# Kernel tuning notes

Hardware: AMD Instinct MI355X
Metric: run time of the kernel (lower is better)

The kernel has to match this reference:

```python
import jax, jax.numpy as jnp
import numpy as np

B, T, D, H = 2, 2048, 1024, 16
HD = D // H


def sinusoidal_rel_pe(seq_len, d_model, dtype=jnp.float32):
    # Relative positions T-1 .. 0 (reversed), standard sin/cos interleave.
    pos = jnp.arange(seq_len - 1, -1, -1, dtype=jnp.float32)[:, None]  # [T,1]
    div = jnp.exp(-jnp.log(jnp.float32(10000.0)) * jnp.arange(0, d_model, 2, dtype=jnp.float32) / d_model)
    pe = jnp.zeros((seq_len, d_model), dtype=jnp.float32)
    pe = pe.at[:, 0::2].set(jnp.sin(pos * div))
    pe = pe.at[:, 1::2].set(jnp.cos(pos * div))
    return pe.astype(dtype)


def relative_to_absolute(x):
    # x: [B,H,T,L] with L == T. Music-Transformer skew trick.
    b, h, t1, l = x.shape
    x = jnp.pad(x, ((0, 0), (0, 0), (0, 0), (1, 0)))          # pad left of last dim
    x = x.reshape(b, h, -1)
    x = jnp.pad(x, ((0, 0), (0, 0), (l - t1, 0)))
    x = x.reshape(b, h, 1 + t1, l)
    return x[:, :, 1:]


def setup_inputs() -> dict:
    key = jax.random.key(0)
    k1, k2, k3 = jax.random.split(key, 3)
    x = jax.random.normal(k1, (B, T, D), dtype=jnp.float32)
    # causal mask: True where attention is disallowed (j > i)
    mask = jnp.triu(jnp.ones((T, T), dtype=bool), k=1)[None, None]
    mask = jnp.broadcast_to(mask, (B, 1, T, T))
    Wqkv = jax.random.normal(k2, (D, 3 * D), dtype=jnp.float32) * 0.02
    Wout = jax.random.normal(k3, (D, D), dtype=jnp.float32) * 0.02
    bout = jnp.zeros((D,), dtype=jnp.float32)
    return {"x": x, "mask": mask, "Wqkv": Wqkv, "Wout": Wout, "bout": bout}


def reference(x, mask, Wqkv, Wout, bout):
    b, t, d = x.shape
    scale = jnp.sqrt(jnp.float32(HD)).astype(x.dtype)
    qkv = x @ Wqkv                                  # [B,T,3D]
    q, k, v = jnp.split(qkv, 3, axis=-1)
    E = sinusoidal_rel_pe(t, d, x.dtype)            # [T,D], constant rel bias
    q = q.reshape(b, t, H, HD).transpose(0, 2, 1, 3)   # [B,H,T,hd]
    k = k.reshape(b, t, H, HD).transpose(0, 2, 1, 3)
    v = v.reshape(b, t, H, HD).transpose(0, 2, 1, 3)
    Eh = E.reshape(t, H, HD).transpose(1, 0, 2)        # [H,T,hd]
    att_k = jnp.einsum('bhqd,bhkd->bhqk', q, k)
    att_e = relative_to_absolute(jnp.einsum('bhqd,hkd->bhqk', q, Eh))
    score = (att_k + att_e) / scale
    score = jnp.where(mask, -jnp.inf, score)
    score = jax.nn.softmax(score, axis=-1)          # dropout is identity (eval)
    ctx = jnp.einsum('bhqk,bhkd->bhqd', score, v)
    ctx = ctx.transpose(0, 2, 1, 3).reshape(b, t, d)
    out = ctx @ Wout + bout
    return (out, score)
```

## Files before the change

### kernel.cpp

```cpp
#include <hip/hip_runtime.h>

typedef __bf16 bf16x8 __attribute__((ext_vector_type(8)));
typedef float f32x4 __attribute__((ext_vector_type(4)));
typedef float f32x16 __attribute__((ext_vector_type(16)));

#define B_ 2
#define T_ 2048
#define D_ 1024
#define H_ 16

__device__ __forceinline__ ushort f2bf(float f) {
  union { float f; unsigned u; } v; v.f = f;
  unsigned u = v.u;
  return (ushort)((u + 0x7FFFu + ((u >> 16) & 1u)) >> 16);
}

__device__ __forceinline__ void g2l16(const void* g, void* l) {
  __builtin_amdgcn_global_load_lds(
      (const __attribute__((address_space(1))) unsigned int*)g,
      (__attribute__((address_space(3))) unsigned int*)l, 16, 0, 0);
}

__global__ __launch_bounds__(256) void cvt_kernel(const float* __restrict__ in,
                                                  ushort* __restrict__ out) {
  int i = (blockIdx.x * 256 + threadIdx.x) * 4;
  float4 v = *(const float4*)(in + i);
  ushort4 o;
  o.x = f2bf(v.x); o.y = f2bf(v.y); o.z = f2bf(v.z); o.w = f2bf(v.w);
  *(ushort4*)(out + i) = o;
}

__global__ void transpose_cvt(const float* __restrict__ in, ushort* __restrict__ out,
                              int R, int C) {
  __shared__ float tile[32][33];
  int bx = blockIdx.x * 32, by = blockIdx.y * 32;
  int tx = threadIdx.x, ty = threadIdx.y;
  for (int i = 0; i < 32; i += 8)
    tile[ty + i][tx] = in[(size_t)(by + ty + i) * C + (bx + tx)];
  __syncthreads();
  for (int i = 0; i < 32; i += 8)
    out[(size_t)(bx + ty + i) * R + (by + tx)] = f2bf(tile[tx][ty + i]);
}

__global__ __launch_bounds__(256) void gemm_bf16(
    const ushort* __restrict__ A, const ushort* __restrict__ BT,
    float* __restrict__ C, const float* __restrict__ bias,
    int M, int N, int K) {
  __shared__ alignas(16) ushort As[2][4096];
  __shared__ alignas(16) ushort Bs[2][4096];
  int tid = threadIdx.x;
  int wave = tid >> 6, lane = tid & 63;
  int l16 = lane & 15, lhi = lane >> 4;
  int m0 = blockIdx.y * 128, n0 = blockIdx.x * 128;
  int wr = (wave >> 1) * 64, wc = (wave & 1) * 64;
  int srow = lane >> 2, sch = lane & 3;

  f32x4 acc[4][4] = {};

  auto stage = [&](int kk, int buf) {
    for (int i = 0; i < 2; ++i) {
      int rg = i * 4 + wave;
      g2l16(A + (size_t)(m0 + rg * 16 + srow) * K + kk + sch * 8, &As[buf][rg * 512]);
      g2l16(BT + (size_t)(n0 + rg * 16 + srow) * K + kk + sch * 8, &Bs[buf][rg * 512]);
    }
  };

  stage(0, 0);
  int buf = 0;
  for (int kk = 0; kk < K; kk += 32) {
    __syncthreads();
    if (kk + 32 < K) stage(kk + 32, buf ^ 1);
    const ushort* Asb = As[buf];
    const ushort* Bsb = Bs[buf];
    bf16x8 af[4], bfr[4];
    for (int f = 0; f < 4; ++f)
      af[f] = *(const bf16x8*)(Asb + (wr + f * 16 + l16) * 32 + lhi * 8);
    for (int f = 0; f < 4; ++f)
      bfr[f] = *(const bf16x8*)(Bsb + (wc + f * 16 + l16) * 32 + lhi * 8);
    for (int fm = 0; fm < 4; ++fm)
      for (int fn = 0; fn < 4; ++fn)
        acc[fm][fn] = __builtin_amdgcn_mfma_f32_16x16x32_bf16(af[fm], bfr[fn], acc[fm][fn], 0, 0, 0);
    buf ^= 1;
  }
  for (int fm = 0; fm < 4; ++fm)
    for (int fn = 0; fn < 4; ++fn)
      for (int r = 0; r < 4; ++r) {
        int row = m0 + wr + fm * 16 + lhi * 4 + r;
        int col = n0 + wc + fn * 16 + l16;
        float v = acc[fm][fn][r];
        if (bias) v += bias[col];
        C[(size_t)row * N + col] = v;
      }
}

__global__ __launch_bounds__(256) void augment_kernel(
    const float* __restrict__ qkv,
    ushort* __restrict__ Qaug, ushort* __restrict__ Kaug, ushort* __restrict__ Vb) {
  int row = blockIdx.x;
  int b = row >> 11;
  int t = row & 2047;
  int tid = threadIdx.x;
  const float* src = qkv + (size_t)row * 3072;
  for (int i = 0; i < 4; ++i) {
    int idx = tid + i * 256;
    int h = idx >> 6, d = idx & 63;
    size_t obase = ((size_t)(b * H_ + h) * T_ + t);
    float q = src[idx];
    float k = src[1024 + idx];
    float v = src[2048 + idx];
    Qaug[obase * 128 + d] = f2bf(q * 0.125f);
    Kaug[obase * 128 + d] = f2bf(k);
    Vb[obase * 64 + d] = f2bf(v);
  }
  for (int i = 0; i < 2; ++i) {
    int idx = tid + i * 256;
    int h = idx >> 5, mm = idx & 31;
    int gdim = h * 64 + 2 * mm;
    float w = __expf(-9.2103403719761836f * (float)gdim * (1.0f / 1024.0f));
    float ang = w * (float)t;
    float si, co;
    __sincosf(ang, &si, &co);
    float qs = src[h * 64 + 2 * mm], qc = src[h * 64 + 2 * mm + 1];
    size_t obase = ((size_t)(b * H_ + h) * T_ + t);
    Qaug[obase * 128 + 64 + 2 * mm]     = f2bf((qs * si + qc * co) * 0.125f);
    Qaug[obase * 128 + 64 + 2 * mm + 1] = f2bf((qc * si - qs * co) * 0.125f);
    Kaug[obase * 128 + 64 + 2 * mm]     = f2bf(co);
    Kaug[obase * 128 + 64 + 2 * mm + 1] = f2bf(si);
  }
}

__global__ __launch_bounds__(256) void transpose_v(const ushort* __restrict__ Vb,
                                                   ushort* __restrict__ Vt) {
  __shared__ ushort tile[64][72];
  int bh = blockIdx.y, t0 = blockIdx.x * 64;
  int tid = threadIdx.x;
  for (int i = 0; i < 2; ++i) {
    int e = tid + i * 256;
    int row = e >> 3, ch = e & 7;
    *(int4*)(&tile[row][ch * 8]) =
        *(const int4*)(Vb + ((size_t)bh * T_ + t0 + row) * 64 + ch * 8);
  }
  __syncthreads();
  for (int i = 0; i < 2; ++i) {
    int e = tid + i * 256;
    int d = e >> 3, ch = e & 7;
    union { int4 v; ushort u[8]; } pk;
    for (int u = 0; u < 8; ++u) pk.u[u] = tile[ch * 8 + u][d];
    *(int4*)(Vt + ((size_t)bh * 64 + d) * T_ + t0 + ch * 8) = pk.v;
  }
}

__device__ __forceinline__ int rowf32(int reg, int hi) {
  return (reg & 3) + 8 * (reg >> 2) + 4 * hi;
}

__global__ __launch_bounds__(256, 4) void denom_kernel(
    const ushort* __restrict__ Qaug,
    const ushort* __restrict__ Kaug,
    float* __restrict__ invlb) {
  int flat = blockIdx.y * 32 + blockIdx.x;
  int wg = (flat & 7) * 128 + (flat >> 3);
  int bh = wg >> 5;
  int qt = 31 - (wg & 31);
  int tid = threadIdx.x;
  int wave = tid >> 6, lane = tid & 63;
  int l31 = lane & 31, hi = lane >> 5;
  int r = wave >> 1, d = wave & 1;

  __shared__ alignas(16) ushort Ks[2][8192];
  __shared__ float sums[64];

  const ushort* Kbase = Kaug + (size_t)bh * T_ * 128;

  auto stageK = [&](int kt, int buf) {
    for (int i = 0; i < 4; ++i) {
      int rg = i * 4 + wave;
      int key = rg * 4 + (lane >> 4);
      const ushort* g = Kbase + ((size_t)(kt * 64 + key)) * 128 + (((lane & 15) ^ (key & 15)) << 3);
      g2l16(g, &Ks[buf][rg * 512]);
    }
  };

  bf16x8 qf[8];
  {
    const ushort* Qg = Qaug + ((size_t)bh * T_ + qt * 64 + r * 32 + l31) * 128;
    for (int ks = 0; ks < 8; ++ks)
      qf[ks] = *(const bf16x8*)(Qg + ks * 16 + hi * 8);
  }
  int key = d * 32 + l31;

  stageK(0, 0);
  asm volatile("s_waitcnt vmcnt(0)" ::: "memory");
  __builtin_amdgcn_s_barrier();
  float plsum[16];
  for (int i = 0; i < 16; ++i) plsum[i] = 0.f;

  for (int kt = 0; kt <= qt; ++kt) {
    int buf = kt & 1;
    if (kt < qt) stageK(kt + 1, buf ^ 1);
    __builtin_amdgcn_sched_barrier(0);
    const ushort* Kb = Ks[buf];
    f32x16 s = {};
    for (int ks = 0; ks < 8; ++ks) {
      int slot = (ks * 2 + hi) ^ (key & 15);
      bf16x8 kf = *(const bf16x8*)(Kb + key * 128 + (slot << 3));
      s = __builtin_amdgcn_mfma_f32_32x32x16_bf16(qf[ks], kf, s, 0, 0, 0);
    }
    if (kt == qt) {
      for (int reg = 0; reg < 16; ++reg)
        if (d * 32 + l31 > r * 32 + rowf32(reg, hi)) s[reg] = -1e30f;
    }
    for (int reg = 0; reg < 16; ++reg) plsum[reg] += __expf(s[reg]);
    if (kt < qt) {
      asm volatile("s_waitcnt vmcnt(0)" ::: "memory");
      __builtin_amdgcn_s_barrier();
    }
  }
  for (int reg = 0; reg < 16; ++reg) {
    float v = plsum[reg];
    for (int dd = 1; dd < 32; dd <<= 1) v += __shfl_xor(v, dd);
    plsum[reg] = v;
  }
  if (d == 1 && l31 == 0)
    for (int reg = 0; reg < 16; ++reg)
      sums[r * 32 + rowf32(reg, hi)] = plsum[reg];
  __syncthreads();
  if (d == 0 && l31 == 0)
    for (int reg = 0; reg < 16; ++reg) {
      int row = r * 32 + rowf32(reg, hi);
      invlb[(size_t)bh * T_ + qt * 64 + row] = 1.f / (plsum[reg] + sums[row]);
    }
}

__global__ __launch_bounds__(256) void attn2_kernel(
    const ushort* __restrict__ Qaug,
    const ushort* __restrict__ Kaug,
    const ushort* __restrict__ Vt,
    const float* __restrict__ invlb,
    float* __restrict__ score,
    ushort* __restrict__ ctxb) {
  int flat = blockIdx.y * 32 + blockIdx.x;
  int wg = (flat & 7) * 128 + (flat >> 3);
  int bh = wg >> 5;
  int qt = 31 - (wg & 31);
  int tid = threadIdx.x;
  int wave = tid >> 6, lane = tid & 63;
  int l31 = lane & 31, hi = lane >> 5;
  int r = wave >> 1, d = wave & 1;

  __shared__ alignas(16) ushort Ks[2][8192];
  __shared__ alignas(16) ushort Vs[2][4096];
  __shared__ alignas(16) ushort Ps[4096];

  const ushort* Kbase = Kaug + (size_t)bh * T_ * 128;
  const ushort* Vbase = Vt + (size_t)bh * 64 * T_;

  auto stageK = [&](int kt, int buf) {
    for (int i = 0; i < 4; ++i) {
      int rg = i * 4 + wave;
      int key = rg * 4 + (lane >> 4);
      const ushort* g = Kbase + ((size_t)(kt * 64 + key)) * 128 + (((lane & 15) ^ (key & 15)) << 3);
      g2l16(g, &Ks[buf][rg * 512]);
    }
  };
  auto stageV = [&](int kt, int buf) {
    for (int i = 0; i < 2; ++i) {
      int rg = i * 4 + wave;
      int dim = rg * 8 + (lane >> 3);
      const ushort* g = Vbase + (size_t)dim * T_ + kt * 64 + (((lane & 7) ^ (dim & 7)) << 3);
      g2l16(g, &Vs[buf][rg * 512]);
    }
  };

  bf16x8 qf[8];
  {
    const ushort* Qg = Qaug + ((size_t)bh * T_ + qt * 64 + r * 32 + l31) * 128;
    for (int ks = 0; ks < 8; ++ks)
      qf[ks] = *(const bf16x8*)(Qg + ks * 16 + hi * 8);
  }
  int key = d * 32 + l31;
  float4 iv[4];
  for (int g = 0; g < 4; ++g)
    iv[g] = *(const float4*)(invlb + (size_t)bh * T_ + qt * 64 + r * 32 + hi * 4 + g * 8);

  stageK(0, 0);
  stageV(0, 0);
  asm volatile("s_waitcnt vmcnt(0)" ::: "memory");
  __builtin_amdgcn_s_barrier();
  f32x16 cacc[2] = {};
  float* srow = score + ((size_t)bh * T_ + (size_t)qt * 64) * T_;

  for (int kt = 0; kt <= qt; ++kt) {
    int buf = kt & 1;
    if (kt < qt) { stageK(kt + 1, buf ^ 1); stageV(kt + 1, buf ^ 1); }
    __builtin_amdgcn_sched_barrier(0);
    const ushort* Kb = Ks[buf];
    f32x16 s = {};
    for (int ks = 0; ks < 8; ++ks) {
      int slot = (ks * 2 + hi) ^ (key & 15);
      bf16x8 kf = *(const bf16x8*)(Kb + key * 128 + (slot << 3));
      s = __builtin_amdgcn_mfma_f32_32x32x16_bf16(qf[ks], kf, s, 0, 0, 0);
    }
    if (kt == qt) {
      for (int reg = 0; reg < 16; ++reg)
        if (d * 32 + l31 > r * 32 + rowf32(reg, hi)) s[reg] = -1e30f;
    }
    for (int reg = 0; reg < 16; ++reg) {
      int row_loc = r * 32 + rowf32(reg, hi);
      float p = __expf(s[reg]) * iv[reg >> 2][reg & 3];
      srow[(size_t)row_loc * T_ + kt * 64 + key] = p;
      Ps[row_loc * 64 + ((((key >> 3)) ^ (row_loc & 7)) << 3) + (key & 7)] = f2bf(p);
    }
    asm volatile("s_waitcnt lgkmcnt(0)" ::: "memory");
    __builtin_amdgcn_sched_barrier(0);
    const ushort* Vb2 = Vs[buf];
    int rowA = r * 32 + l31;
    for (int ks2 = 0; ks2 < 2; ++ks2) {
      int chunkA = d * 4 + ks2 * 2 + hi;
      bf16x8 pa = *(const bf16x8*)(Ps + rowA * 64 + ((chunkA ^ (rowA & 7)) << 3));
      for (int b2 = 0; b2 < 2; ++b2) {
        int dim = b2 * 32 + l31;
        bf16x8 vb = *(const bf16x8*)(Vb2 + dim * 64 + ((chunkA ^ (dim & 7)) << 3));
        cacc[b2] = __builtin_amdgcn_mfma_f32_32x32x16_bf16(pa, vb, cacc[b2], 0, 0, 0);
      }
    }
    if (kt < qt) {
      asm volatile("s_waitcnt vmcnt(16)" ::: "memory");
      __builtin_amdgcn_s_barrier();
    }
  }

  {
    int row = tid >> 2, c16 = (tid & 3) * 16;
    f32x4 z = {0.f, 0.f, 0.f, 0.f};
    for (int kt = qt + 1; kt < 32; ++kt) {
      f32x4* dst = (f32x4*)(srow + (size_t)row * T_ + kt * 64 + c16);
      for (int u = 0; u < 4; ++u) dst[u] = z;
    }
  }

  __builtin_amdgcn_s_barrier();
  float* xch = (float*)Ks;
  if (d == 1) {
    for (int b2 = 0; b2 < 2; ++b2)
      for (int reg = 0; reg < 16; ++reg)
        xch[(r * 32 + rowf32(reg, hi)) * 64 + b2 * 32 + l31] = cacc[b2][reg];
  }
  __syncthreads();
  if (d == 0) {
    int b = bh >> 4, h = bh & 15;
    for (int b2 = 0; b2 < 2; ++b2)
      for (int reg = 0; reg < 16; ++reg) {
        int row_loc = r * 32 + rowf32(reg, hi);
        float v = cacc[b2][reg] + xch[row_loc * 64 + b2 * 32 + l31];
        int t = qt * 64 + row_loc;
        ctxb[((size_t)(b * T_ + t)) * 1024 + h * 64 + b2 * 32 + l31] = f2bf(v);
      }
  }
}

extern "C" void kernel_launch(void* const* d_in, const int* in_sizes, int n_in,
                              void* d_out, int out_size, void* d_ws, size_t ws_size,
                              hipStream_t stream) {
  const float* x    = (const float*)d_in[0];
  const float* Wqkv = (const float*)d_in[2];
  const float* Wout = (const float*)d_in[3];
  const float* bout = (const float*)d_in[4];

  char* ws = (char*)d_ws;
  ushort* xb    = (ushort*)(ws + 0);
  ushort* wqkvT = (ushort*)(ws + 8388608);
  ushort* woutT = (ushort*)(ws + 14680064);
  float*  qkv   = (float*) (ws + 16777216);
  ushort* Qaug  = (ushort*)(ws + 67108864);
  ushort* Kaug  = (ushort*)(ws + 83886080);
  ushort* Vb    = (ushort*)(ws + 100663296);
  ushort* ctxb  = (ushort*)(ws + 109051904);
  ushort* Vt    = (ushort*)(ws + 16777216);
  float*  invlb = (float*) (ws + 25165824);

  float* out   = (float*)d_out;
  float* score = out + (size_t)4194304;

  cvt_kernel<<<4096, 256, 0, stream>>>(x, xb);
  dim3 tb(32, 8);
  transpose_cvt<<<dim3(3072 / 32, 1024 / 32), tb, 0, stream>>>(Wqkv, wqkvT, 1024, 3072);
  transpose_cvt<<<dim3(1024 / 32, 1024 / 32), tb, 0, stream>>>(Wout, woutT, 1024, 1024);
  gemm_bf16<<<dim3(24, 32), 256, 0, stream>>>(xb, wqkvT, qkv, nullptr, 4096, 3072, 1024);
  augment_kernel<<<4096, 256, 0, stream>>>(qkv, Qaug, Kaug, Vb);
  transpose_v<<<dim3(32, 32), 256, 0, stream>>>(Vb, Vt);
  denom_kernel<<<dim3(32, 32), 256, 0, stream>>>(Qaug, Kaug, invlb);
  attn2_kernel<<<dim3(32, 32), 256, 0, stream>>>(Qaug, Kaug, Vt, invlb, score, ctxb);
  gemm_bf16<<<dim3(8, 32), 256, 0, stream>>>(ctxb, woutT, out, bout, 4096, 1024, 1024);
}
```

Before: 315.2 us.

## Fuse QKV augmentation into GEMM epilogue and precompute K trig columns

The QKV GEMM now writes bf16 Q (scaled, with the rotated relative-position half computed via shuffle-paired sin/cos), K and V directly in a token-major [B,T,H,128] layout. This removes the fp32 qkv intermediate and the separate augment kernel. A small kernel fills K's cos/sin columns independently of the GEMM. The attention kernels are re-indexed to read the new strided layout, so each K/Q row load now has a 4 KB stride between tokens instead of a contiguous per-head stream, and the GEMM epilogue takes on scattered 2-byte stores and sincos work.

```diff
diff --git a/kernel.cpp b/kernel.cpp
--- a/kernel.cpp
+++ b/kernel.cpp
@@ -8,6 +8,7 @@
 #define T_ 2048
 #define D_ 1024
 #define H_ 16
+#define NLOG4 -9.2103403719761836f
 
 __device__ __forceinline__ ushort f2bf(float f) {
   union { float f; unsigned u; } v; v.f = f;
@@ -42,10 +43,22 @@
     out[(size_t)(bx + ty + i) * R + (by + tx)] = f2bf(tile[tx][ty + i]);
 }
 
-__global__ __launch_bounds__(256) void gemm_bf16(
+__global__ __launch_bounds__(512) void fill_ktrig(ushort* __restrict__ Ka) {
+  int t = blockIdx.x;
+  int tid = threadIdx.x;
+  int h = tid >> 5, mm = tid & 31;
+  float w = __expf(NLOG4 * (float)(h * 64 + 2 * mm) * (1.0f / 1024.0f));
+  float si, co;
+  __sincosf(w * (float)t, &si, &co);
+  ushort2 pk;
+  pk.x = f2bf(co); pk.y = f2bf(si);
+  for (int b = 0; b < 2; ++b)
+    *(ushort2*)(Ka + ((size_t)(b * T_ + t) * 2048 + h * 128 + 64 + 2 * mm)) = pk;
+}
+
+__global__ __launch_bounds__(256) void gemm_qkv(
     const ushort* __restrict__ A, const ushort* __restrict__ BT,
-    float* __restrict__ C, const float* __restrict__ bias,
-    int M, int N, int K) {
+    ushort* __restrict__ Qa, ushort* __restrict__ Ka, ushort* __restrict__ Va) {
   __shared__ alignas(16) ushort As[2][4096];
   __shared__ alignas(16) ushort Bs[2][4096];
   int tid = threadIdx.x;
@@ -54,6 +67,7 @@
   int m0 = blockIdx.y * 128, n0 = blockIdx.x * 128;
   int wr = (wave >> 1) * 64, wc = (wave & 1) * 64;
   int srow = lane >> 2, sch = lane & 3;
+  const int K = 1024;
 
   f32x4 acc[4][4] = {};
 
@@ -82,6 +96,77 @@
         acc[fm][fn] = __builtin_amdgcn_mfma_f32_16x16x32_bf16(af[fm], bfr[fn], acc[fm][fn], 0, 0, 0);
     buf ^= 1;
   }
+
+  int slice = n0 >> 10;
+  bool odd = l16 & 1;
+  for (int fn = 0; fn < 4; ++fn) {
+    int col = n0 + wc + fn * 16 + l16;
+    int d = col & 1023;
+    int h = d >> 6, hd = d & 63;
+    float w = (slice == 0) ? __expf(NLOG4 * (float)(d & ~1) * (1.0f / 1024.0f)) : 0.f;
+    for (int fm = 0; fm < 4; ++fm) {
+      int row0 = m0 + wr + fm * 16 + lhi * 4;
+      int t0 = row0 & 2047;
+      for (int r = 0; r < 4; ++r) {
+        size_t row = (size_t)(row0 + r);
+        float v = acc[fm][fn][r];
+        if (slice == 0) {
+          float prt = __shfl_xor(v, 1);
+          float si, co;
+          __sincosf(w * (float)(t0 + r), &si, &co);
+          float tr = odd ? (v * si - prt * co) : (v * si + prt * co);
+          Qa[row * 2048 + h * 128 + hd] = f2bf(v * 0.125f);
+          Qa[row * 2048 + h * 128 + 64 + hd] = f2bf(tr * 0.125f);
+        } else if (slice == 1) {
+          Ka[row * 2048 + h * 128 + hd] = f2bf(v);
+        } else {
+          Va[row * 1024 + h * 64 + hd] = f2bf(v);
+        }
+      }
+    }
+  }
+}
+
+__global__ __launch_bounds__(256) void gemm_bf16(
+    const ushort* __restrict__ A, const ushort* __restrict__ BT,
+    float* __restrict__ C, const float* __restrict__ bias,
+    int M, int N, int K) {
+  __shared__ alignas(16) ushort As[2][4096];
+  __shared__ alignas(16) ushort Bs[2][4096];
+  int tid = threadIdx.x;
+  int wave = tid >> 6, lane = tid & 63;
+  int l16 = lane & 15, lhi = lane >> 4;
+  int m0 = blockIdx.y * 128, n0 = blockIdx.x * 128;
+  int wr = (wave >> 1) * 64, wc = (wave & 1) * 64;
+  int srow = lane >> 2, sch = lane & 3;
+
+  f32x4 acc[4][4] = {};
+
+  auto stage = [&](int kk, int buf) {
+    for (int i = 0; i < 2; ++i) {
+      int rg = i * 4 + wave;
+      g2l16(A + (size_t)(m0 + rg * 16 + srow) * K + kk + sch * 8, &As[buf][rg * 512]);
+      g2l16(BT + (size_t)(n0 + rg * 16 + srow) * K + kk + sch * 8, &Bs[buf][rg * 512]);
+    }
+  };
+
+  stage(0, 0);
+  int buf = 0;
+  for (int kk = 0; kk < K; kk += 32) {
+    __syncthreads();
+    if (kk + 32 < K) stage(kk + 32, buf ^ 1);
+    const ushort* Asb = As[buf];
+    const ushort* Bsb = Bs[buf];
+    bf16x8 af[4], bfr[4];
+    for (int f = 0; f < 4; ++f)
+      af[f] = *(const bf16x8*)(Asb + (wr + f * 16 + l16) * 32 + lhi * 8);
+    for (int f = 0; f < 4; ++f)
+      bfr[f] = *(const bf16x8*)(Bsb + (wc + f * 16 + l16) * 32 + lhi * 8);
+    for (int fm = 0; fm < 4; ++fm)
+      for (int fn = 0; fn < 4; ++fn)
+        acc[fm][fn] = __builtin_amdgcn_mfma_f32_16x16x32_bf16(af[fm], bfr[fn], acc[fm][fn], 0, 0, 0);
+    buf ^= 1;
+  }
   for (int fm = 0; fm < 4; ++fm)
     for (int fn = 0; fn < 4; ++fn)
       for (int r = 0; r < 4; ++r) {
@@ -93,52 +178,17 @@
       }
 }
 
-__global__ __launch_bounds__(256) void augment_kernel(
-    const float* __restrict__ qkv,
-    ushort* __restrict__ Qaug, ushort* __restrict__ Kaug, ushort* __restrict__ Vb) {
-  int row = blockIdx.x;
-  int b = row >> 11;
-  int t = row & 2047;
-  int tid = threadIdx.x;
-  const float* src = qkv + (size_t)row * 3072;
-  for (int i = 0; i < 4; ++i) {
-    int idx = tid + i * 256;
-    int h = idx >> 6, d = idx & 63;
-    size_t obase = ((size_t)(b * H_ + h) * T_ + t);
-    float q = src[idx];
-    float k = src[1024 + idx];
-    float v = src[2048 + idx];
-    Qaug[obase * 128 + d] = f2bf(q * 0.125f);
-    Kaug[obase * 128 + d] = f2bf(k);
-    Vb[obase * 64 + d] = f2bf(v);
-  }
-  for (int i = 0; i < 2; ++i) {
-    int idx = tid + i * 256;
-    int h = idx >> 5, mm = idx & 31;
-    int gdim = h * 64 + 2 * mm;
-    float w = __expf(-9.2103403719761836f * (float)gdim * (1.0f / 1024.0f));
-    float ang = w * (float)t;
-    float si, co;
-    __sincosf(ang, &si, &co);
-    float qs = src[h * 64 + 2 * mm], qc = src[h * 64 + 2 * mm + 1];
-    size_t obase = ((size_t)(b * H_ + h) * T_ + t);
-    Qaug[obase * 128 + 64 + 2 * mm]     = f2bf((qs * si + qc * co) * 0.125f);
-    Qaug[obase * 128 + 64 + 2 * mm + 1] = f2bf((qc * si - qs * co) * 0.125f);
-    Kaug[obase * 128 + 64 + 2 * mm]     = f2bf(co);
-    Kaug[obase * 128 + 64 + 2 * mm + 1] = f2bf(si);
-  }
-}
-
-__global__ __launch_bounds__(256) void transpose_v(const ushort* __restrict__ Vb,
+__global__ __launch_bounds__(256) void transpose_v(const ushort* __restrict__ Va,
                                                    ushort* __restrict__ Vt) {
   __shared__ ushort tile[64][72];
   int bh = blockIdx.y, t0 = blockIdx.x * 64;
+  int b = bh >> 4, h = bh & 15;
   int tid = threadIdx.x;
   for (int i = 0; i < 2; ++i) {
     int e = tid + i * 256;
     int row = e >> 3, ch = e & 7;
     *(int4*)(&tile[row][ch * 8]) =
-        *(const int4*)(Vb + ((size_t)bh * T_ + t0 + row) * 64 + ch * 8);
+        *(const int4*)(Va + ((size_t)(b * T_ + t0 + row)) * 1024 + h * 64 + ch * 8);
   }
   __syncthreads();
   for (int i = 0; i < 2; ++i) {
@@ -155,13 +205,14 @@
 }
 
 __global__ __launch_bounds__(256, 4) void denom_kernel(
-    const ushort* __restrict__ Qaug,
-    const ushort* __restrict__ Kaug,
+    const ushort* __restrict__ Qa,
+    const ushort* __restrict__ Ka,
     float* __restrict__ invlb) {
   int flat = blockIdx.y * 32 + blockIdx.x;
   int wg = (flat & 7) * 128 + (flat >> 3);
   int bh = wg >> 5;
   int qt = 31 - (wg & 31);
+  int bb = bh >> 4, hh = bh & 15;
   int tid = threadIdx.x;
   int wave = tid >> 6, lane = tid & 63;
   int l31 = lane & 31, hi = lane >> 5;
@@ -169,21 +220,20 @@
 
   __shared__ alignas(16) ushort Ks[2][8192];
   __shared__ float sums[64];
-
-  const ushort* Kbase = Kaug + (size_t)bh * T_ * 128;
 
   auto stageK = [&](int kt, int buf) {
     for (int i = 0; i < 4; ++i) {
       int rg = i * 4 + wave;
       int key = rg * 4 + (lane >> 4);
-      const ushort* g = Kbase + ((size_t)(kt * 64 + key)) * 128 + (((lane & 15) ^ (key & 15)) << 3);
+      const ushort* g = Ka + ((size_t)(bb * T_ + kt * 64 + key)) * 2048 + hh * 128 +
+                        (((lane & 15) ^ (key & 15)) << 3);
       g2l16(g, &Ks[buf][rg * 512]);
     }
   };
 
   bf16x8 qf[8];
   {
-    const ushort* Qg = Qaug + ((size_t)bh * T_ + qt * 64 + r * 32 + l31) * 128;
+    const ushort* Qg = Qa + ((size_t)(bb * T_ + qt * 64 + r * 32 + l31)) * 2048 + hh * 128;
     for (int ks = 0; ks < 8; ++ks)
       qf[ks] = *(const bf16x8*)(Qg + ks * 16 + hi * 8);
   }
@@ -233,8 +283,8 @@
 }
 
 __global__ __launch_bounds__(256) void attn2_kernel(
-    const ushort* __restrict__ Qaug,
-    const ushort* __restrict__ Kaug,
+    const ushort* __restrict__ Qa,
+    const ushort* __restrict__ Ka,
     const ushort* __restrict__ Vt,
     const float* __restrict__ invlb,
     float* __restrict__ score,
@@ -243,6 +293,7 @@
   int wg = (flat & 7) * 128 + (flat >> 3);
   int bh = wg >> 5;
   int qt = 31 - (wg & 31);
+  int bb = bh >> 4, hh = bh & 15;
   int tid = threadIdx.x;
   int wave = tid >> 6, lane = tid & 63;
   int l31 = lane & 31, hi = lane >> 5;
@@ -252,14 +303,14 @@
   __shared__ alignas(16) ushort Vs[2][4096];
   __shared__ alignas(16) ushort Ps[4096];
 
-  const ushort* Kbase = Kaug + (size_t)bh * T_ * 128;
   const ushort* Vbase = Vt + (size_t)bh * 64 * T_;
 
   auto stageK = [&](int kt, int buf) {
     for (int i = 0; i < 4; ++i) {
       int rg = i * 4 + wave;
       int key = rg * 4 + (lane >> 4);
-      const ushort* g = Kbase + ((size_t)(kt * 64 + key)) * 128 + (((lane & 15) ^ (key & 15)) << 3);
+      const ushort* g = Ka + ((size_t)(bb * T_ + kt * 64 + key)) * 2048 + hh * 128 +
+                        (((lane & 15) ^ (key & 15)) << 3);
       g2l16(g, &Ks[buf][rg * 512]);
     }
   };
@@ -274,7 +325,7 @@
 
   bf16x8 qf[8];
   {
-    const ushort* Qg = Qaug + ((size_t)bh * T_ + qt * 64 + r * 32 + l31) * 128;
+    const ushort* Qg = Qa + ((size_t)(bb * T_ + qt * 64 + r * 32 + l31)) * 2048 + hh * 128;
     for (int ks = 0; ks < 8; ++ks)
       qf[ks] = *(const bf16x8*)(Qg + ks * 16 + hi * 8);
   }
@@ -348,13 +399,12 @@
   }
   __syncthreads();
   if (d == 0) {
-    int b = bh >> 4, h = bh & 15;
     for (int b2 = 0; b2 < 2; ++b2)
       for (int reg = 0; reg < 16; ++reg) {
         int row_loc = r * 32 + rowf32(reg, hi);
         float v = cacc[b2][reg] + xch[row_loc * 64 + b2 * 32 + l31];
         int t = qt * 64 + row_loc;
-        ctxb[((size_t)(b * T_ + t)) * 1024 + h * 64 + b2 * 32 + l31] = f2bf(v);
+        ctxb[((size_t)(bb * T_ + t)) * 1024 + hh * 64 + b2 * 32 + l31] = f2bf(v);
       }
   }
 }
@@ -371,13 +421,12 @@
   ushort* xb    = (ushort*)(ws + 0);
   ushort* wqkvT = (ushort*)(ws + 8388608);
   ushort* woutT = (ushort*)(ws + 14680064);
-  float*  qkv   = (float*) (ws + 16777216);
-  ushort* Qaug  = (ushort*)(ws + 67108864);
-  ushort* Kaug  = (ushort*)(ws + 83886080);
-  ushort* Vb    = (ushort*)(ws + 100663296);
-  ushort* ctxb  = (ushort*)(ws + 109051904);
-  ushort* Vt    = (ushort*)(ws + 16777216);
-  float*  invlb = (float*) (ws + 25165824);
+  ushort* Qa    = (ushort*)(ws + 16777216);
+  ushort* Ka    = (ushort*)(ws + 33554432);
+  ushort* Va    = (ushort*)(ws + 50331648);
+  ushort* Vt    = (ushort*)(ws + 58720256);
+  ushort* ctxb  = (ushort*)(ws + 67108864);
+  float*  invlb = (float*) (ws + 75497472);
 
   float* out   = (float*)d_out;
   float* score = out + (size_t)4194304;
@@ -386,10 +435,10 @@
   dim3 tb(32, 8);
   transpose_cvt<<<dim3(3072 / 32, 1024 / 32), tb, 0, stream>>>(Wqkv, wqkvT, 1024, 3072);
   transpose_cvt<<<dim3(1024 / 32, 1024 / 32), tb, 0, stream>>>(Wout, woutT, 1024, 1024);
-  gemm_bf16<<<dim3(24, 32), 256, 0, stream>>>(xb, wqkvT, qkv, nullptr, 4096, 3072, 1024);
-  augment_kernel<<<4096, 256, 0, stream>>>(qkv, Qaug, Kaug, Vb);
-  transpose_v<<<dim3(32, 32), 256, 0, stream>>>(Vb, Vt);
-  denom_kernel<<<dim3(32, 32), 256, 0, stream>>>(Qaug, Kaug, invlb);
-  attn2_kernel<<<dim3(32, 32), 256, 0, stream>>>(Qaug, Kaug, Vt, invlb, score, ctxb);
+  fill_ktrig<<<2048, 512, 0, stream>>>(Ka);
+  gemm_qkv<<<dim3(24, 32), 256, 0, stream>>>(xb, wqkvT, Qa, Ka, Va);
+  transpose_v<<<dim3(32, 32), 256, 0, stream>>>(Va, Vt);
+  denom_kernel<<<dim3(32, 32), 256, 0, stream>>>(Qa, Ka, invlb);
+  attn2_kernel<<<dim3(32, 32), 256, 0, stream>>>(Qa, Ka, Vt, invlb, score, ctxb);
   gemm_bf16<<<dim3(8, 32), 256, 0, stream>>>(ctxb, woutT, out, bout, 4096, 1024, 1024);
 }
```

After: 685.2 us. 2.17x slower.
